# Optimization experiments

Hardware: AMD Instinct MI355X
Metric: run time of the kernel (lower is better)

## Reference

```python
import jax, jax.numpy as jnp
import numpy as np
import math

EPS = 1e-3  # numerical_stabilizer in relu_kernel_transformation


def setup_inputs() -> dict:
    key = jax.random.key(0)
    ks = jax.random.split(key, 6)
    B, L, DIM = 8, 4096, 768
    H, D, M = 12, 64, 256
    x = jax.random.normal(ks[0], (B, L, DIM), dtype=jnp.float32)
    qkv_w = jax.random.normal(ks[1], (3 * DIM, DIM), dtype=jnp.float32) * (DIM ** -0.5)
    qkv_b = jnp.zeros((3 * DIM,), dtype=jnp.float32)
    proj_w = jax.random.normal(ks[2], (DIM, DIM), dtype=jnp.float32) * (DIM ** -0.5)
    proj_b = jnp.zeros((DIM,), dtype=jnp.float32)
    # Gaussian orthogonal random matrix [M, D] (blocks of orthogonal rows, chi-scaled)
    blocks = []
    for i in range(M // D):
        g = jax.random.normal(ks[3 + 0] if False else jax.random.fold_in(ks[3], i), (D, D), dtype=jnp.float32)
        q, _ = jnp.linalg.qr(g)
        blocks.append(q.T)
    pm = jnp.concatenate(blocks, axis=0)  # [M, D]
    mult = jnp.linalg.norm(jax.random.normal(ks[4], (M, D), dtype=jnp.float32), axis=1)
    proj_mat = mult[:, None] * pm
    return {"x": x, "qkv_w": qkv_w, "qkv_b": qkv_b,
            "proj_w": proj_w, "proj_b": proj_b, "proj_mat": proj_mat}


def _relu_features(t, proj_mat):
    # t: [B, L, H, D], proj_mat: [M, D] -> [B, L, H, M]
    ratio = 1.0 / math.sqrt(float(proj_mat.shape[0]))
    z = ratio * jnp.einsum('blhd,md->blhm', t, proj_mat)
    return jax.nn.relu(z) + EPS


def reference(x, qkv_w, qkv_b, proj_w, proj_b, proj_mat):
    B, L, DIM = x.shape
    H = 12
    D = DIM // H
    qkv = x @ qkv_w.T + qkv_b                      # [B, L, 3*DIM]
    qkv = qkv.reshape(B, L, 3, H, D)
    q, k, v = qkv[:, :, 0], qkv[:, :, 1], qkv[:, :, 2]   # [B, L, H, D]
    q_p = _relu_features(q, proj_mat)              # [B, L, H, M]
    k_p = _relu_features(k, proj_mat)              # [B, L, H, M]
    # Non-causal FAVOR+ linear attention
    kv = jnp.einsum('blhm,blhd->bhmd', k_p, v)     # [B, H, M, D]
    k_sum = k_p.sum(axis=1)                        # [B, H, M]
    num = jnp.einsum('blhm,bhmd->blhd', q_p, kv)   # [B, L, H, D]
    den = jnp.einsum('blhm,bhm->blh', q_p, k_sum)  # [B, L, H]
    out = num / den[..., None]
    out = out.reshape(B, L, DIM)
    return out @ proj_w.T + proj_b
```

## Files before the change

kernel.cpp:

```cpp
#include <hip/hip_runtime.h>
#include <hip/hip_bf16.h>
#include <cstdint>

typedef __hip_bfloat16 bf16;
typedef short bf16x8 __attribute__((ext_vector_type(8)));
typedef float f32x4 __attribute__((ext_vector_type(4)));

#define RATIO 0.0625f
#define EPS_F 0.001f

__device__ __forceinline__ void unpack8(uint4 u, float* f) {
  f[0] = __uint_as_float(u.x << 16); f[1] = __uint_as_float(u.x & 0xffff0000u);
  f[2] = __uint_as_float(u.y << 16); f[3] = __uint_as_float(u.y & 0xffff0000u);
  f[4] = __uint_as_float(u.z << 16); f[5] = __uint_as_float(u.z & 0xffff0000u);
  f[6] = __uint_as_float(u.w << 16); f[7] = __uint_as_float(u.w & 0xffff0000u);
}

__device__ __forceinline__ unsigned short f2bf(float f) {
  unsigned int u = __float_as_uint(f);
  unsigned int r = (u + 0x7fffu + ((u >> 16) & 1u)) >> 16;
  return (unsigned short)r;
}

__device__ __forceinline__ void gload_lds16(const void* g, void* l) {
  __builtin_amdgcn_global_load_lds(
      (const __attribute__((address_space(1))) void*)(uintptr_t)g,
      (__attribute__((address_space(3))) void*)(uintptr_t)l, 16, 0, 0);
}

__global__ void zero_kernel(float* __restrict__ p, int n) {
  int i = blockIdx.x * 256 + threadIdx.x;
  if (i < n) p[i] = 0.f;
}

__global__ void conv_kernel(const float* __restrict__ src,
                            unsigned short* __restrict__ dst, long n) {
  long i = ((long)blockIdx.x * 256 + threadIdx.x) * 4;
  if (i < n) {
    float4 v = *(const float4*)(src + i);
    ushort4 o;
    o.x = f2bf(v.x); o.y = f2bf(v.y); o.z = f2bf(v.z); o.w = f2bf(v.w);
    *(ushort4*)(dst + i) = o;
  }
}

template <bool OUT_F32>
__global__ __launch_bounds__(256) void gemm_bt_kernel(
    const bf16* __restrict__ A, const bf16* __restrict__ Bt,
    const float* __restrict__ bias, void* __restrict__ Cout,
    int Ndim, int Kdim)
{
  __shared__ short As[128 * 32];
  __shared__ short Bs[128 * 32];
  int tid = threadIdx.x;
  int lane = tid & 63;
  int wave = tid >> 6;
  int wm = (wave >> 1) * 64;
  int wn = (wave & 1) * 64;
  long m0 = (long)blockIdx.y * 128;
  long n0 = (long)blockIdx.x * 128;

  int g_row = wave * 32 + (lane >> 2);
  int g_col = (lane & 3) * 8;
  const bf16* Ag = A + (m0 + g_row) * (long)Kdim + g_col;
  const bf16* Bg = Bt + (n0 + g_row) * (long)Kdim + g_col;
  short* Ad = &As[(wave * 32) * 32];
  short* Bd = &Bs[(wave * 32) * 32];

  f32x4 acc[4][4];
#pragma unroll
  for (int i = 0; i < 4; i++)
#pragma unroll
    for (int j = 0; j < 4; j++)
      acc[i][j] = (f32x4){0.f, 0.f, 0.f, 0.f};

  int mrow = lane & 15;
  int kq = (lane >> 4) * 8;

  for (int k0 = 0; k0 < Kdim; k0 += 32) {
    __syncthreads();
    gload_lds16(Ag + k0,             Ad);
    gload_lds16(Ag + k0 + 16 * (long)Kdim, Ad + 16 * 32);
    gload_lds16(Bg + k0,             Bd);
    gload_lds16(Bg + k0 + 16 * (long)Kdim, Bd + 16 * 32);
    __syncthreads();
    bf16x8 af[4], bfr[4];
#pragma unroll
    for (int mi = 0; mi < 4; mi++)
      af[mi] = *(const bf16x8*)&As[(wm + mi * 16 + mrow) * 32 + kq];
#pragma unroll
    for (int ni = 0; ni < 4; ni++)
      bfr[ni] = *(const bf16x8*)&Bs[(wn + ni * 16 + mrow) * 32 + kq];
#pragma unroll
    for (int mi = 0; mi < 4; mi++)
#pragma unroll
      for (int ni = 0; ni < 4; ni++)
        acc[mi][ni] = __builtin_amdgcn_mfma_f32_16x16x32_bf16(af[mi], bfr[ni], acc[mi][ni], 0, 0, 0);
  }

#pragma unroll
  for (int ni = 0; ni < 4; ni++) {
    long col = n0 + wn + ni * 16 + (lane & 15);
    float bv = bias[col];
#pragma unroll
    for (int mi = 0; mi < 4; mi++) {
      long row = m0 + wm + mi * 16 + (lane >> 4) * 4;
#pragma unroll
      for (int r = 0; r < 4; r++) {
        float val = acc[mi][ni][r] + bv;
        if (OUT_F32)
          ((float*)Cout)[(row + r) * Ndim + col] = val;
        else
          ((bf16*)Cout)[(row + r) * Ndim + col] = __float2bfloat16(val);
      }
    }
  }
}

__global__ __launch_bounds__(256) void kv_mfma_kernel(
    const bf16* __restrict__ qkv, const bf16* __restrict__ pmb,
    float* __restrict__ kvbuf, float* __restrict__ ksumb)
{
  int bh = blockIdx.x;
  int b = bh / 12, h = bh % 12;
  int l0 = blockIdx.y * 1024;
  int tid = threadIdx.x, lane = tid & 63, w = tid >> 6;
  int quad = lane >> 4, l16 = lane & 15;

  __shared__ short k_lds[64 * 72];
  __shared__ short v_lds[64 * 72];
  __shared__ short kp3[256 * 72];

  f32x4 kvacc[4][4];
#pragma unroll
  for (int mt = 0; mt < 4; mt++)
#pragma unroll
    for (int dt = 0; dt < 4; dt++)
      kvacc[mt][dt] = (f32x4){0.f, 0.f, 0.f, 0.f};
  float ksum_r = 0.f;

  int srow = tid >> 2, sseg = (tid & 3) * 8;
  int swz = ((srow >> 3) & 3) << 4;

  for (int tile = 0; tile < 16; tile++) {
    long gr = ((long)(b * 4096 + l0 + tile * 64 + srow)) * 2304 + h * 64;
    uint4 kk0 = *(const uint4*)(qkv + gr + 768 + sseg);
    uint4 kk1 = *(const uint4*)(qkv + gr + 768 + sseg + 32);
    uint4 vv0 = *(const uint4*)(qkv + gr + 1536 + sseg);
    uint4 vv1 = *(const uint4*)(qkv + gr + 1536 + sseg + 32);
    __syncthreads();
    *(uint4*)&k_lds[srow * 72 + sseg] = kk0;
    *(uint4*)&k_lds[srow * 72 + sseg + 32] = kk1;
    *(uint4*)&v_lds[srow * 72 + (sseg ^ swz)] = vv0;
    *(uint4*)&v_lds[srow * 72 + ((sseg + 32) ^ swz)] = vv1;
    __syncthreads();

    bf16x8 af[4][2], bpm[4][2];
#pragma unroll
    for (int lt = 0; lt < 4; lt++)
#pragma unroll
      for (int ks = 0; ks < 2; ks++)
        af[lt][ks] = *(const bf16x8*)&k_lds[(lt * 16 + l16) * 72 + ks * 32 + quad * 8];
#pragma unroll
    for (int mt = 0; mt < 4; mt++)
#pragma unroll
      for (int ks = 0; ks < 2; ks++)
        bpm[mt][ks] = *(const bf16x8*)(pmb + (w * 64 + mt * 16 + l16) * 64 + ks * 32 + quad * 8);

#pragma unroll
    for (int lt = 0; lt < 4; lt++)
#pragma unroll
      for (int mt = 0; mt < 4; mt++) {
        f32x4 s = (f32x4){0.f, 0.f, 0.f, 0.f};
        s = __builtin_amdgcn_mfma_f32_16x16x32_bf16(af[lt][0], bpm[mt][0], s, 0, 0, 0);
        s = __builtin_amdgcn_mfma_f32_16x16x32_bf16(af[lt][1], bpm[mt][1], s, 0, 0, 0);
        ushort4 pk;
        pk.x = f2bf(fmaxf(s[0] * RATIO, 0.f) + EPS_F);
        pk.y = f2bf(fmaxf(s[1] * RATIO, 0.f) + EPS_F);
        pk.z = f2bf(fmaxf(s[2] * RATIO, 0.f) + EPS_F);
        pk.w = f2bf(fmaxf(s[3] * RATIO, 0.f) + EPS_F);
        *(ushort4*)&kp3[(w * 64 + mt * 16 + l16) * 72 + lt * 16 + quad * 4] = pk;
      }
    __syncthreads();

#pragma unroll
    for (int j8 = 0; j8 < 8; j8++) {
      uint4 u = *(const uint4*)&kp3[tid * 72 + j8 * 8];
      float f[8]; unpack8(u, f);
      ksum_r += ((f[0] + f[1]) + (f[2] + f[3])) + ((f[4] + f[5]) + (f[6] + f[7]));
    }

#pragma unroll
    for (int ls = 0; ls < 2; ls++) {
      bf16x8 a2[4];
#pragma unroll
      for (int mt = 0; mt < 4; mt++)
        a2[mt] = *(const bf16x8*)&kp3[(w * 64 + mt * 16 + l16) * 72 + ls * 32 + quad * 8];
#pragma unroll
      for (int dt = 0; dt < 4; dt++) {
        bf16x8 b2;
        int dcol = (dt * 16 + l16) ^ (quad << 4);
#pragma unroll
        for (int jj = 0; jj < 8; jj++)
          b2[jj] = v_lds[(ls * 32 + quad * 8 + jj) * 72 + dcol];
#pragma unroll
        for (int mt = 0; mt < 4; mt++)
          kvacc[mt][dt] = __builtin_amdgcn_mfma_f32_16x16x32_bf16(a2[mt], b2, kvacc[mt][dt], 0, 0, 0);
      }
    }
  }

#pragma unroll
  for (int mt = 0; mt < 4; mt++)
#pragma unroll
    for (int dt = 0; dt < 4; dt++)
#pragma unroll
      for (int r = 0; r < 4; r++)
        atomicAdd(kvbuf + ((long)bh * 64 + dt * 16 + l16) * 256 + w * 64 + mt * 16 + quad * 4 + r,
                  kvacc[mt][dt][r]);
  atomicAdd(ksumb + bh * 256 + tid, ksum_r);
}

__global__ __launch_bounds__(256) void attn_mfma_kernel(
    const bf16* __restrict__ qkv, const bf16* __restrict__ pmb,
    const bf16* __restrict__ kvtb, const float* __restrict__ ksumb,
    bf16* __restrict__ attn)
{
  int bh = blockIdx.x;
  int b = bh / 12, h = bh % 12;
  int l0 = blockIdx.y * 64;
  int tid = threadIdx.x, lane = tid & 63, w = tid >> 6;
  int quad = lane >> 4, l16 = lane & 15;

  __shared__ short q_lds[64 * 72];
  __shared__ short qp2[64 * 264];
  __shared__ short kvt_lds[64 * 264];
  __shared__ float ksum_lds[256];
  __shared__ float den_part[4][64];

  {
    int srow = tid >> 2, sseg = (tid & 3) * 8;
    long gr = ((long)(b * 4096 + l0 + srow)) * 2304 + h * 64;
    *(uint4*)&q_lds[srow * 72 + sseg]      = *(const uint4*)(qkv + gr + sseg);
    *(uint4*)&q_lds[srow * 72 + sseg + 32] = *(const uint4*)(qkv + gr + sseg + 32);
  }
  {
    int row = tid >> 2, cb = (tid & 3) * 64;
    const bf16* src = kvtb + (long)bh * 16384 + row * 256 + cb;
    short* dst = &kvt_lds[row * 264 + cb];
#pragma unroll
    for (int j = 0; j < 8; j++)
      *(uint4*)(dst + j * 8) = *(const uint4*)(src + j * 8);
  }
  ksum_lds[tid] = ksumb[bh * 256 + tid];
  __syncthreads();

  {
    bf16x8 apm[4][2], bq[4][2];
#pragma unroll
    for (int mt = 0; mt < 4; mt++)
#pragma unroll
      for (int ks = 0; ks < 2; ks++)
        apm[mt][ks] = *(const bf16x8*)(pmb + (w * 64 + mt * 16 + l16) * 64 + ks * 32 + quad * 8);
#pragma unroll
    for (int lt = 0; lt < 4; lt++)
#pragma unroll
      for (int ks = 0; ks < 2; ks++)
        bq[lt][ks] = *(const bf16x8*)&q_lds[(lt * 16 + l16) * 72 + ks * 32 + quad * 8];

#pragma unroll
    for (int mt = 0; mt < 4; mt++)
#pragma unroll
      for (int lt = 0; lt < 4; lt++) {
        f32x4 s = (f32x4){0.f, 0.f, 0.f, 0.f};
        s = __builtin_amdgcn_mfma_f32_16x16x32_bf16(apm[mt][0], bq[lt][0], s, 0, 0, 0);
        s = __builtin_amdgcn_mfma_f32_16x16x32_bf16(apm[mt][1], bq[lt][1], s, 0, 0, 0);
        ushort4 pk;
        pk.x = f2bf(fmaxf(s[0] * RATIO, 0.f) + EPS_F);
        pk.y = f2bf(fmaxf(s[1] * RATIO, 0.f) + EPS_F);
        pk.z = f2bf(fmaxf(s[2] * RATIO, 0.f) + EPS_F);
        pk.w = f2bf(fmaxf(s[3] * RATIO, 0.f) + EPS_F);
        *(ushort4*)&qp2[(lt * 16 + l16) * 264 + w * 64 + mt * 16 + quad * 4] = pk;
      }
  }
  __syncthreads();

  {
    int l = tid & 63, Q = tid >> 6;
    float dp = 0.f;
#pragma unroll
    for (int j8 = 0; j8 < 8; j8++) {
      uint4 u = *(const uint4*)&qp2[l * 264 + Q * 64 + j8 * 8];
      float f[8]; unpack8(u, f);
#pragma unroll
      for (int i = 0; i < 8; i++) dp += f[i] * ksum_lds[Q * 64 + j8 * 8 + i];
    }
    den_part[Q][l] = dp;
  }

  f32x4 o[4];
#pragma unroll
  for (int dt = 0; dt < 4; dt++) o[dt] = (f32x4){0.f, 0.f, 0.f, 0.f};
#pragma unroll
  for (int ms = 0; ms < 8; ms++) {
    bf16x8 aq = *(const bf16x8*)&qp2[(w * 16 + l16) * 264 + ms * 32 + quad * 8];
#pragma unroll
    for (int dt = 0; dt < 4; dt++) {
      bf16x8 bk = *(const bf16x8*)&kvt_lds[(dt * 16 + l16) * 264 + ms * 32 + quad * 8];
      o[dt] = __builtin_amdgcn_mfma_f32_16x16x32_bf16(aq, bk, o[dt], 0, 0, 0);
    }
  }
  __syncthreads();

  float rden[4];
#pragma unroll
  for (int r = 0; r < 4; r++) {
    int l = w * 16 + quad * 4 + r;
    rden[r] = 1.f / (den_part[0][l] + den_part[1][l] + den_part[2][l] + den_part[3][l]);
  }
#pragma unroll
  for (int dt = 0; dt < 4; dt++)
#pragma unroll
    for (int r = 0; r < 4; r++) {
      int l = w * 16 + quad * 4 + r;
      attn[((long)(b * 4096 + l0 + l)) * 768 + h * 64 + dt * 16 + l16] =
          __float2bfloat16(o[dt][r] * rden[r]);
    }
}

extern "C" void kernel_launch(void* const* d_in, const int* in_sizes, int n_in,
                              void* d_out, int out_size, void* d_ws, size_t ws_size,
                              hipStream_t stream)
{
  const float* x      = (const float*)d_in[0];
  const float* qkv_w  = (const float*)d_in[1];
  const float* qkv_b  = (const float*)d_in[2];
  const float* proj_w = (const float*)d_in[3];
  const float* proj_b = (const float*)d_in[4];
  const float* pmat   = (const float*)d_in[5];
  float* out = (float*)d_out;

  char* ws = (char*)d_ws;
  bf16*  qkv   = (bf16*)ws;
  bf16*  xbuf  = (bf16*)(ws + 150994944);
  bf16*  attn  = xbuf;
  float* kvbuf = (float*)(ws + 201326592);
  float* ksumb = (float*)(ws + 207618048);
  bf16*  wqkv  = (bf16*)(ws + 207716352);
  bf16*  kvtb  = (bf16*)(ws + 207716352);
  bf16*  pmb   = (bf16*)(ws + 210862080);
  bf16*  wproj = (bf16*)(ws + 211255296);

  int nz = 96 * 64 * 256 + 96 * 256;
  zero_kernel<<<dim3((nz + 255) / 256), 256, 0, stream>>>(kvbuf, nz);

  conv_kernel<<<dim3(25165824 / 1024), 256, 0, stream>>>(x, (unsigned short*)xbuf, 25165824L);
  conv_kernel<<<dim3(1769472 / 1024), 256, 0, stream>>>(qkv_w, (unsigned short*)wqkv, 1769472L);
  conv_kernel<<<dim3(589824 / 1024), 256, 0, stream>>>(proj_w, (unsigned short*)wproj, 589824L);

  gemm_bt_kernel<false><<<dim3(2304 / 128, 32768 / 128), 256, 0, stream>>>(
      xbuf, wqkv, qkv_b, qkv, 2304, 768);

  conv_kernel<<<dim3(16384 / 1024), 256, 0, stream>>>(pmat, (unsigned short*)pmb, 16384L);

  kv_mfma_kernel<<<dim3(96, 4), 256, 0, stream>>>(qkv, pmb, kvbuf, ksumb);

  conv_kernel<<<dim3(1572864 / 1024), 256, 0, stream>>>(kvbuf, (unsigned short*)kvtb, 1572864L);

  attn_mfma_kernel<<<dim3(96, 64), 256, 0, stream>>>(qkv, pmb, kvtb, ksumb, attn);

  gemm_bt_kernel<true><<<dim3(768 / 128, 32768 / 128), 256, 0, stream>>>(
      attn, wproj, proj_b, out, 768, 768);
}
```

Baseline: 621.5 us.

## Rewrite GEMM as 256x256 double-buffered, swizzled, XCD-remapped pipelined kernel

The bf16 GEMM kernel moves from 128x128 tiles with a K-step of 32 to 256x256 tiles with a K-step of 64, run by 512 threads. LDS is double-buffered, with global-to-LDS prefetch of the next K slice interleaved with MFMA phases. An XOR swizzle on the LDS layout avoids bank conflicts, and workgroups are remapped so each XCD gets a contiguous chunk. The goal is to hide memory latency and raise MFMA utilisation for both projection GEMMs. The cost is heavy LDS use (128KB) and a large accumulator register footprint. The manual waitcnt/barrier choreography is fragile, and the 256 tile needs dimensions to divide evenly.

```diff
diff --git a/kernel.cpp b/kernel.cpp
--- a/kernel.cpp
+++ b/kernel.cpp
@@ -44,69 +44,176 @@
   }
 }
 
+__device__ __forceinline__ void ds_read_B8(const short* Bb, int rB0, int l16,
+                                           int quad, bf16x8 bfr[4][2]) {
+  const int sw = l16 & 7;
+#pragma unroll
+  for (int ni = 0; ni < 4; ++ni)
+#pragma unroll
+    for (int ks = 0; ks < 2; ++ks)
+      bfr[ni][ks] = *(const bf16x8*)
+          &Bb[(rB0 + ni * 16 + l16) * 64 + (((ks * 4 + quad) ^ sw) * 8)];
+}
+
+template <int Q>
+__device__ __forceinline__ void ds_read_A4(const short* Ab, int l16, int quad,
+                                           bf16x8 af[2][2]) {
+  const int sw = l16 & 7;
+#pragma unroll
+  for (int i = 0; i < 2; ++i)
+#pragma unroll
+    for (int ks = 0; ks < 2; ++ks)
+      af[i][ks] = *(const bf16x8*)
+          &Ab[((Q * 2 + i) * 16 + l16) * 64 + (((ks * 4 + quad) ^ sw) * 8)];
+}
+
+template <int Q>
+__device__ __forceinline__ void mfma16(f32x4 acc[8][4], bf16x8 af[2][2],
+                                       bf16x8 bfr[4][2]) {
+#pragma unroll
+  for (int i = 0; i < 2; ++i)
+#pragma unroll
+    for (int ni = 0; ni < 4; ++ni)
+#pragma unroll
+      for (int ks = 0; ks < 2; ++ks)
+        acc[Q * 2 + i][ni] = __builtin_amdgcn_mfma_f32_16x16x32_bf16(
+            af[i][ks], bfr[ni][ks], acc[Q * 2 + i][ni], 0, 0, 0);
+}
+
 template <bool OUT_F32>
-__global__ __launch_bounds__(256) void gemm_bt_kernel(
+__global__ __launch_bounds__(512, 2) void gemm_bt_kernel(
     const bf16* __restrict__ A, const bf16* __restrict__ Bt,
     const float* __restrict__ bias, void* __restrict__ Cout,
     int Ndim, int Kdim)
 {
-  __shared__ short As[128 * 32];
-  __shared__ short Bs[128 * 32];
-  int tid = threadIdx.x;
-  int lane = tid & 63;
-  int wave = tid >> 6;
-  int wm = (wave >> 1) * 64;
-  int wn = (wave & 1) * 64;
-  long m0 = (long)blockIdx.y * 128;
-  long n0 = (long)blockIdx.x * 128;
-
-  int g_row = wave * 32 + (lane >> 2);
-  int g_col = (lane & 3) * 8;
-  const bf16* Ag = A + (m0 + g_row) * (long)Kdim + g_col;
-  const bf16* Bg = Bt + (n0 + g_row) * (long)Kdim + g_col;
-  short* Ad = &As[(wave * 32) * 32];
-  short* Bd = &Bs[(wave * 32) * 32];
-
-  f32x4 acc[4][4];
-#pragma unroll
-  for (int i = 0; i < 4; i++)
+  __shared__ short lds[65536];
+  const int tid = threadIdx.x;
+  const int lane = tid & 63;
+  const int w = tid >> 6;
+  const int wr = w >> 2;
+  const int wc = w & 3;
+  const int quad = lane >> 4, l16 = lane & 15;
+
+  int gx = gridDim.x;
+  int nwg = gx * gridDim.y;
+  int flat = blockIdx.y * gx + blockIdx.x;
+  int qq = nwg >> 3, rr = nwg & 7;
+  int xcd = flat & 7, sub = flat >> 3;
+  int wg = (xcd < rr ? xcd * (qq + 1) : rr * (qq + 1) + (xcd - rr) * qq) + sub;
+  long m0 = (long)(wg / gx) * 256;
+  long n0 = (long)(wg % gx) * 256;
+
+  const int r8 = lane >> 3;
+  const int csw = ((lane & 7) ^ (r8 & 7)) * 8;
+  const bf16* gAs = A + (m0 + (w >> 2) * 128 + (w & 3) * 8 + r8) * (long)Kdim + csw;
+  const bf16* gBs = Bt + (n0 + w * 8 + r8) * (long)Kdim + csw;
+  short* dA = &lds[(w >> 2) * 8192 + (w & 3) * 512];
+  short* dB = &lds[32768 + w * 512];
+  const long kb64 = 64L * Kdim;
+  const long ka32 = 32L * Kdim;
+
+  f32x4 acc[8][4];
+#pragma unroll
+  for (int i = 0; i < 8; i++)
 #pragma unroll
     for (int j = 0; j < 4; j++)
       acc[i][j] = (f32x4){0.f, 0.f, 0.f, 0.f};
 
-  int mrow = lane & 15;
-  int kq = (lane >> 4) * 8;
-
-  for (int k0 = 0; k0 < Kdim; k0 += 32) {
-    __syncthreads();
-    gload_lds16(Ag + k0,             Ad);
-    gload_lds16(Ag + k0 + 16 * (long)Kdim, Ad + 16 * 32);
-    gload_lds16(Bg + k0,             Bd);
-    gload_lds16(Bg + k0 + 16 * (long)Kdim, Bd + 16 * 32);
-    __syncthreads();
-    bf16x8 af[4], bfr[4];
-#pragma unroll
-    for (int mi = 0; mi < 4; mi++)
-      af[mi] = *(const bf16x8*)&As[(wm + mi * 16 + mrow) * 32 + kq];
-#pragma unroll
-    for (int ni = 0; ni < 4; ni++)
-      bfr[ni] = *(const bf16x8*)&Bs[(wn + ni * 16 + mrow) * 32 + kq];
-#pragma unroll
-    for (int mi = 0; mi < 4; mi++)
-#pragma unroll
-      for (int ni = 0; ni < 4; ni++)
-        acc[mi][ni] = __builtin_amdgcn_mfma_f32_16x16x32_bf16(af[mi], bfr[ni], acc[mi][ni], 0, 0, 0);
-  }
-
-#pragma unroll
-  for (int ni = 0; ni < 4; ni++) {
-    long col = n0 + wn + ni * 16 + (lane & 15);
+  const int NIT = Kdim >> 6;
+
+#pragma unroll
+  for (int j = 0; j < 4; ++j) gload_lds16(gBs + j * kb64, dB + j * 4096);
+#pragma unroll
+  for (int qa = 0; qa < 4; ++qa) gload_lds16(gAs + qa * ka32, dA + qa * 2048);
+  asm volatile("s_waitcnt vmcnt(3)" ::: "memory");
+  __builtin_amdgcn_s_barrier();
+
+  bf16x8 bfr[4][2], af[2][2];
+
+  for (int it = 0; it < NIT; ++it) {
+    const int d = it & 1, nd = d ^ 1;
+    const bool pf = (it < NIT - 1);
+    const long kq1 = (long)(it + 1) * 64;
+    const short* Ab = &lds[d * 16384 + wr * 8192];
+    const short* Bb = &lds[32768 + d * 16384 + (wc >> 1) * 8192];
+    const int rB0 = (wc & 1) * 64;
+    short* dAn = dA + nd * 16384;
+    short* dBn = dB + nd * 16384;
+
+    ds_read_B8(Bb, rB0, l16, quad, bfr);
+    ds_read_A4<0>(Ab, l16, quad, af);
+    if (pf) {
+      gload_lds16(gBs + kq1, dBn);
+      gload_lds16(gBs + kb64 + kq1, dBn + 4096);
+      asm volatile("s_waitcnt vmcnt(4)" ::: "memory");
+    } else {
+      asm volatile("s_waitcnt vmcnt(2)" ::: "memory");
+    }
+    asm volatile("s_waitcnt lgkmcnt(8)" ::: "memory");
+    __builtin_amdgcn_s_barrier();
+    asm volatile("s_waitcnt lgkmcnt(0)" ::: "memory");
+    __builtin_amdgcn_sched_barrier(0);
+    __builtin_amdgcn_s_setprio(1);
+    mfma16<0>(acc, af, bfr);
+    __builtin_amdgcn_s_setprio(0);
+    __builtin_amdgcn_s_barrier();
+
+    ds_read_A4<1>(Ab, l16, quad, af);
+    if (pf) {
+      gload_lds16(gBs + 2 * kb64 + kq1, dBn + 8192);
+      gload_lds16(gBs + 3 * kb64 + kq1, dBn + 12288);
+      asm volatile("s_waitcnt vmcnt(5)" ::: "memory");
+    } else {
+      asm volatile("s_waitcnt vmcnt(1)" ::: "memory");
+    }
+    __builtin_amdgcn_s_barrier();
+    asm volatile("s_waitcnt lgkmcnt(0)" ::: "memory");
+    __builtin_amdgcn_sched_barrier(0);
+    __builtin_amdgcn_s_setprio(1);
+    mfma16<1>(acc, af, bfr);
+    __builtin_amdgcn_s_setprio(0);
+    __builtin_amdgcn_s_barrier();
+
+    ds_read_A4<2>(Ab, l16, quad, af);
+    if (pf) {
+      gload_lds16(gAs + kq1, dAn);
+      gload_lds16(gAs + ka32 + kq1, dAn + 2048);
+      asm volatile("s_waitcnt vmcnt(6)" ::: "memory");
+    } else {
+      asm volatile("s_waitcnt vmcnt(0)" ::: "memory");
+    }
+    __builtin_amdgcn_s_barrier();
+    asm volatile("s_waitcnt lgkmcnt(0)" ::: "memory");
+    __builtin_amdgcn_sched_barrier(0);
+    __builtin_amdgcn_s_setprio(1);
+    mfma16<2>(acc, af, bfr);
+    __builtin_amdgcn_s_setprio(0);
+    __builtin_amdgcn_s_barrier();
+
+    ds_read_A4<3>(Ab, l16, quad, af);
+    if (pf) {
+      gload_lds16(gAs + 2 * ka32 + kq1, dAn + 4096);
+      gload_lds16(gAs + 3 * ka32 + kq1, dAn + 6144);
+      asm volatile("s_waitcnt vmcnt(3)" ::: "memory");
+    }
+    __builtin_amdgcn_s_barrier();
+    asm volatile("s_waitcnt lgkmcnt(0)" ::: "memory");
+    __builtin_amdgcn_sched_barrier(0);
+    __builtin_amdgcn_s_setprio(1);
+    mfma16<3>(acc, af, bfr);
+    __builtin_amdgcn_s_setprio(0);
+    __builtin_amdgcn_s_barrier();
+  }
+
+#pragma unroll
+  for (int ni = 0; ni < 4; ++ni) {
+    long col = n0 + wc * 64 + ni * 16 + l16;
     float bv = bias[col];
 #pragma unroll
-    for (int mi = 0; mi < 4; mi++) {
-      long row = m0 + wm + mi * 16 + (lane >> 4) * 4;
-#pragma unroll
-      for (int r = 0; r < 4; r++) {
+    for (int mi = 0; mi < 8; ++mi) {
+      long row = m0 + wr * 128 + mi * 16 + quad * 4;
+#pragma unroll
+      for (int r = 0; r < 4; ++r) {
         float val = acc[mi][ni][r] + bv;
         if (OUT_F32)
           ((float*)Cout)[(row + r) * Ndim + col] = val;
@@ -358,7 +465,7 @@
   conv_kernel<<<dim3(1769472 / 1024), 256, 0, stream>>>(qkv_w, (unsigned short*)wqkv, 1769472L);
   conv_kernel<<<dim3(589824 / 1024), 256, 0, stream>>>(proj_w, (unsigned short*)wproj, 589824L);
 
-  gemm_bt_kernel<false><<<dim3(2304 / 128, 32768 / 128), 256, 0, stream>>>(
+  gemm_bt_kernel<false><<<dim3(2304 / 256, 32768 / 256), 512, 0, stream>>>(
       xbuf, wqkv, qkv_b, qkv, 2304, 768);
 
   conv_kernel<<<dim3(16384 / 1024), 256, 0, stream>>>(pmat, (unsigned short*)pmb, 16384L);
@@ -369,6 +476,6 @@
 
   attn_mfma_kernel<<<dim3(96, 64), 256, 0, stream>>>(qkv, pmb, kvtb, ksumb, attn);
 
-  gemm_bt_kernel<true><<<dim3(768 / 128, 32768 / 128), 256, 0, stream>>>(
+  gemm_bt_kernel<true><<<dim3(768 / 256, 32768 / 256), 512, 0, stream>>>(
       attn, wproj, proj_b, out, 768, 768);
 }
```

New measurement: 609.5 us. No clear change (-1.9%).
